# Kernel optimization log

Measured on AMD Instinct MI355X. Metric: run time of the kernel, lower is better.

## Reference

```python
import jax, jax.numpy as jnp
import numpy as np

B, TOK, NT = 64, 64, 456          # batch, token_encoder_dim, num gene tokens
T = NT * TOK                      # flat gene_exp dim = 29184
D, H, NL = 256, 8, 4              # d_model, nhead, num_layers
HD = D // H                       # head_dim = 32
FF = 4 * D                        # ffn hidden
PH = 32                           # attention-pooling hidden
L = NT + 1                        # seq len incl. CLS token
LN_EPS = 1e-5
BN_EPS = 1e-5


def build_alibi_slopes(n_heads):
    # faithful to FlashAttentionBlock.build_alibi_slopes (base=2.0)
    return jnp.array([1.0 / 2.0 ** (i // (n_heads / 2.0)) for i in range(n_heads)],
                     dtype=jnp.float32)


def _ln(x, g, b):
    m = jnp.mean(x, axis=-1, keepdims=True)
    v = jnp.mean(jnp.square(x - m), axis=-1, keepdims=True)
    return (x - m) * jax.lax.rsqrt(v + LN_EPS) * g + b


def setup_inputs() -> dict:
    key = jax.random.key(0)
    ks = jax.random.split(key, 24)
    s = 0.02
    return {
        "gene_exp": jax.random.normal(ks[0], (B, T), dtype=jnp.float32),
        "coords": jax.random.normal(ks[1], (B, 3), dtype=jnp.float32),
        "w_in": jax.random.normal(ks[2], (TOK, D)) * s,
        "b_in": jnp.zeros((D,), jnp.float32),
        "w_cls": jax.random.normal(ks[3], (3, D)) * s,
        "b_cls": jnp.zeros((D,), jnp.float32),
        "qkv_w": jax.random.normal(ks[4], (NL, D, 3 * D)) * s,
        "qkv_b": jnp.zeros((NL, 3 * D), jnp.float32),
        "ln1_g": jnp.ones((NL, D), jnp.float32),
        "ln1_b": jnp.zeros((NL, D), jnp.float32),
        "ffn_w1": jax.random.normal(ks[5], (NL, D, FF)) * s,
        "ffn_b1": jnp.zeros((NL, FF), jnp.float32),
        "ffn_w2": jax.random.normal(ks[6], (NL, FF, D)) * s,
        "ffn_b2": jnp.zeros((NL, D), jnp.float32),
        "ln2_g": jnp.ones((NL, D), jnp.float32),
        "ln2_b": jnp.zeros((NL, D), jnp.float32),
        "th1_w": jax.random.normal(ks[7], (D, PH)) * s,
        "th1_b": jnp.zeros((PH,), jnp.float32),
        "bn_g": jnp.ones((PH,), jnp.float32),
        "bn_b": jnp.zeros((PH,), jnp.float32),
        "th2_w": jax.random.normal(ks[8], (PH, 1)) * s,
        "th2_b": jnp.zeros((1,), jnp.float32),
    }


def reference(gene_exp, coords, w_in, b_in, w_cls, b_cls, qkv_w, qkv_b,
              ln1_g, ln1_b, ffn_w1, ffn_b1, ffn_w2, ffn_b2, ln2_g, ln2_b,
              th1_w, th1_b, bn_g, bn_b, th2_w, th2_b):
    # tokenize gene expression + project
    x = gene_exp.reshape(B, NT, TOK) @ w_in + b_in            # [B, NT, D]
    cls = (coords @ w_cls + b_cls)[:, None, :]                # [B, 1, D]
    x = jnp.concatenate([cls, x], axis=1)                     # [B, L, D]

    # ALiBi bias: -slope_h * |i - j| (non-causal flash-attn convention)
    slopes = build_alibi_slopes(H)                            # [H]
    pos = jnp.arange(L, dtype=jnp.float32)
    bias = -slopes[:, None, None] * jnp.abs(pos[:, None] - pos[None, :])  # [H,L,L]

    scale = 1.0 / np.sqrt(HD)
    for l in range(NL):
        residual = x
        qkv = (x @ qkv_w[l] + qkv_b[l]).reshape(B, L, 3, H, HD)
        q, k, v = qkv[:, :, 0], qkv[:, :, 1], qkv[:, :, 2]    # [B, L, H, HD]
        scores = jnp.einsum('bihd,bjhd->bhij', q, k) * scale + bias
        attn = jax.nn.softmax(scores, axis=-1)                # [B, H, L, L]
        out = jnp.einsum('bhij,bjhd->bihd', attn, v).reshape(B, L, D)
        x = _ln(residual + out, ln1_g[l], ln1_b[l])
        residual = x
        h = jax.nn.relu(x @ ffn_w1[l] + ffn_b1[l]) @ ffn_w2[l] + ffn_b2[l]
        x = _ln(residual + h, ln2_g[l], ln2_b[l])

    # AttentionPooling (BatchNorm1d in eval mode: running mean 0, var 1)
    h = x @ th1_w + th1_b                                     # [B, L, PH]
    h = h * (bn_g / np.sqrt(1.0 + BN_EPS)) + bn_b
    scores = jax.nn.gelu(h) @ th2_w + th2_b                   # [B, L, 1]
    attn_w = jax.nn.softmax(scores, axis=1)[..., 0]           # [B, L]
    pooled = jnp.einsum('bl,bld->bd', attn_w, x)              # [B, D]
    return pooled
```

## Files before the change

kernel.cpp:

```cpp
#include <hip/hip_runtime.h>
#include <math.h>

#define B_   64
#define TOK_ 64
#define NT_  456
#define L_   457
#define D_   256
#define H_   8
#define HD_  32
#define FF_  1024
#define NL_  4
#define PH_  32
#define MPAD 29440

typedef unsigned int uint;
typedef unsigned short ushort;
typedef __bf16 v8bf __attribute__((ext_vector_type(8)));
typedef __bf16 v4bf __attribute__((ext_vector_type(4)));
typedef short v4s __attribute__((ext_vector_type(4)));
typedef float v4f __attribute__((ext_vector_type(4)));

__device__ __forceinline__ float bu2f(ushort x) {
    return __uint_as_float(((uint)x) << 16);
}
__device__ __forceinline__ ushort f2bu(float f) {
    union { float f; uint u; } x; x.f = f;
    uint r = (x.u + 0x7fffu + ((x.u >> 16) & 1u)) >> 16;
    return (ushort)r;
}
__device__ __forceinline__ uint pack_bf2(float a, float b) {
#if defined(__HIP_DEVICE_COMPILE__) && __has_builtin(__builtin_amdgcn_cvt_pk_bf16_f32)
    typedef __bf16 bf2v __attribute__((ext_vector_type(2)));
    bf2v v = __builtin_amdgcn_cvt_pk_bf16_f32(a, b);
    return *(uint*)&v;
#else
    return (uint)f2bu(a) | ((uint)f2bu(b) << 16);
#endif
}

__device__ __forceinline__ v4f mfma16(uint2 a, uint2 b, v4f c) {
#if defined(__HIP_DEVICE_COMPILE__)
#if __has_builtin(__builtin_amdgcn_mfma_f32_16x16x16_bf16)
    return __builtin_amdgcn_mfma_f32_16x16x16_bf16(*(v4bf*)&a, *(v4bf*)&b, c, 0, 0, 0);
#else
    return __builtin_amdgcn_mfma_f32_16x16x16bf16_1k(*(v4s*)&a, *(v4s*)&b, c, 0, 0, 0);
#endif
#else
    (void)a; (void)b;
    return c;
#endif
}

__device__ __forceinline__ void gload16(const void* g, void* l) {
    __builtin_amdgcn_global_load_lds(
        (const __attribute__((address_space(1))) void*)(unsigned long long)(uintptr_t)g,
        (__attribute__((address_space(3))) void*)(uint)(uintptr_t)l,
        16, 0, 0);
}

__global__ __launch_bounds__(512, 2) void mfma_gemm8(
    const ushort* __restrict__ A, const ushort* __restrict__ WT,
    const float* __restrict__ bias, ushort* __restrict__ Cout,
    int N, int K, int relu)
{
    __shared__ ushort lds[36864];

    const int NK = K >> 5;

    int nwg = gridDim.x, orig = blockIdx.x;
    int qd = nwg >> 3, rd = nwg & 7;
    int xcd = orig & 7, wi = orig >> 3;
    int wgid = (xcd < rd ? xcd * (qd + 1) : rd * (qd + 1) + (xcd - rd) * qd) + wi;
    int nCB = N >> 7;
    int colblk = (wgid % nCB) << 7;
    int rowblk = (wgid / nCB) << 8;

    int tid = threadIdx.x;
    int wave = tid >> 6, lane = tid & 63;
    int wm = wave >> 1, wn = wave & 1;
    int fr = lane & 15, fq = lane >> 4;

    const ushort* srcA0; const ushort* srcA1; const ushort* srcB0;
    {
        int idx = tid;
        int c = idx >> 3, G = (idx & 7) ^ (c & 7);
        srcA0 = A + (size_t)(rowblk + c * 2 + (G >> 2)) * K + (G & 3) * 8;
        idx = 512 + tid;
        c = idx >> 3; G = (idx & 7) ^ (c & 7);
        srcA1 = A + (size_t)(rowblk + c * 2 + (G >> 2)) * K + (G & 3) * 8;
        idx = tid;
        c = idx >> 3; G = (idx & 7) ^ (c & 7);
        srcB0 = WT + (size_t)(colblk + c * 2 + (G >> 2)) * K + (G & 3) * 8;
    }
    int duA0 = (wave * 64) * 8;
    int duA1 = (512 + wave * 64) * 8;
    int duB  = (wave * 64) * 8;

    int aoff[4], boff[4];
#pragma unroll
    for (int i = 0; i < 4; ++i) {
        int rl = wm * 64 + i * 16 + fr;
        int c = rl >> 1;
        aoff[i] = c * 64 + ((((rl & 1) * 4 + fq) ^ (c & 7)) * 8);
        rl = wn * 64 + i * 16 + fr;
        c = rl >> 1;
        boff[i] = c * 64 + ((((rl & 1) * 4 + fq) ^ (c & 7)) * 8);
    }

    v4f acc[4][4];
#pragma unroll
    for (int i = 0; i < 4; ++i)
#pragma unroll
        for (int j = 0; j < 4; ++j) acc[i][j] = (v4f)0.0f;

#pragma unroll
    for (int t = 0; t < 2; ++t) {
        ushort* pa = lds + t * 8192;
        ushort* pb = lds + 24576 + t * 4096;
        gload16(srcA0 + t * 32, pa + duA0);
        gload16(srcA1 + t * 32, pa + duA1);
        gload16(srcB0 + t * 32, pb + duB);
    }

    for (int t = 0; t < NK; ++t) {
        int slot = t % 3, pslot = (t + 2) % 3;
        const ushort* As = lds + slot * 8192;
        const ushort* Bs = lds + 24576 + slot * 4096;

        if (t < NK - 1) asm volatile("s_waitcnt vmcnt(3)" ::: "memory");
        else            asm volatile("s_waitcnt vmcnt(0)" ::: "memory");
        __builtin_amdgcn_s_barrier();
        asm volatile("" ::: "memory");

        if (t + 2 < NK) {
            ushort* pa = lds + pslot * 8192;
            ushort* pb = lds + 24576 + pslot * 4096;
            gload16(srcA0 + (t + 2) * 32, pa + duA0);
            gload16(srcA1 + (t + 2) * 32, pa + duA1);
            gload16(srcB0 + (t + 2) * 32, pb + duB);
        }

        v8bf av[4], bw[4];
#pragma unroll
        for (int i = 0; i < 4; ++i) av[i] = *(const v8bf*)(As + aoff[i]);
#pragma unroll
        for (int i = 0; i < 4; ++i) bw[i] = *(const v8bf*)(Bs + boff[i]);

        __builtin_amdgcn_s_setprio(1);
#pragma unroll
        for (int mi = 0; mi < 4; ++mi)
#pragma unroll
            for (int ni = 0; ni < 4; ++ni)
                acc[mi][ni] = __builtin_amdgcn_mfma_f32_16x16x32_bf16(
                    av[mi], bw[ni], acc[mi][ni], 0, 0, 0);
        __builtin_amdgcn_s_setprio(0);
    }

    __syncthreads();
    {
        const int PIT = 136;
#pragma unroll
        for (int ni = 0; ni < 4; ++ni) {
            int col = wn * 64 + ni * 16 + fr;
            float bv = bias[colblk + col];
#pragma unroll
            for (int mi = 0; mi < 4; ++mi) {
                int row0 = wm * 64 + mi * 16 + fq * 4;
#pragma unroll
                for (int r2 = 0; r2 < 4; ++r2) {
                    float v = acc[mi][ni][r2] + bv;
                    if (relu) v = fmaxf(v, 0.f);
                    lds[(row0 + r2) * PIT + col] = f2bu(v);
                }
            }
        }
        __syncthreads();
#pragma unroll
        for (int i = 0; i < 8; ++i) {
            int u = tid + 512 * i;
            int row = u >> 4, c8 = (u & 15) * 8;
            uint4 val = *(const uint4*)&lds[row * PIT + c8];
            *(uint4*)(Cout + (size_t)(rowblk + row) * N + colblk + c8) = val;
        }
    }
}

__global__ __launch_bounds__(512, 4) void ffn_kernel(
    const ushort* __restrict__ Xres, const ushort* __restrict__ AO,
    const float* __restrict__ l1g, const float* __restrict__ l1b,
    const ushort* __restrict__ W1P, const ushort* __restrict__ W2P,
    const float* __restrict__ b1, const float* __restrict__ b2,
    const float* __restrict__ l2g, const float* __restrict__ l2b,
    ushort* __restrict__ Xout)
{
    __shared__ ushort Xs[16384];
    __shared__ ushort Hs[64 * 264];

    int r0 = blockIdx.x * 64;
    int tid = threadIdx.x;
    int wave = tid >> 6, lane = tid & 63;
    int fr = lane & 15, fq = lane >> 4;

    {
        float4 g1 = *(const float4*)(l1g + lane * 4);
        float4 be1 = *(const float4*)(l1b + lane * 4);
        ushort4 xr[8], ar[8];
#pragma unroll
        for (int rr = 0; rr < 8; ++rr) {
            size_t off = (size_t)(r0 + wave * 8 + rr) * 256 + lane * 4;
            xr[rr] = *(const ushort4*)(Xres + off);
            ar[rr] = *(const ushort4*)(AO + off);
        }
#pragma unroll
        for (int rr = 0; rr < 8; ++rr) {
            int row = wave * 8 + rr;
            float4 v;
            v.x = bu2f(xr[rr].x) + bu2f(ar[rr].x);
            v.y = bu2f(xr[rr].y) + bu2f(ar[rr].y);
            v.z = bu2f(xr[rr].z) + bu2f(ar[rr].z);
            v.w = bu2f(xr[rr].w) + bu2f(ar[rr].w);
            float s = v.x + v.y + v.z + v.w;
#pragma unroll
            for (int o = 1; o < 64; o <<= 1) s += __shfl_xor(s, o);
            float mean = s * (1.0f / 256.0f);
            float4 d;
            d.x = v.x - mean; d.y = v.y - mean; d.z = v.z - mean; d.w = v.w - mean;
            float sq = d.x * d.x + d.y * d.y + d.z * d.z + d.w * d.w;
#pragma unroll
            for (int o = 1; o < 64; o <<= 1) sq += __shfl_xor(sq, o);
            float rstd = rsqrtf(sq * (1.0f / 256.0f) + 1e-5f);
            ushort4 hb;
            hb.x = f2bu(d.x * rstd * g1.x + be1.x);
            hb.y = f2bu(d.y * rstd * g1.y + be1.y);
            hb.z = f2bu(d.z * rstd * g1.z + be1.z);
            hb.w = f2bu(d.w * rstd * g1.w + be1.w);
            int kt = lane >> 3, g = (lane >> 1) & 3, c = row >> 1;
            int Gp = ((row & 1) * 4 + g) ^ (c & 7);
            int addr = kt * 2048 + (c * 8 + Gp) * 8 + (lane & 1) * 4;
            *(uint2*)&Xs[addr] = *(uint2*)&hb;
        }
    }

    int aoffs[4];
#pragma unroll
    for (int mi = 0; mi < 4; ++mi) {
        int ar2 = mi * 16 + fr, c = ar2 >> 1;
        aoffs[mi] = c * 64 + ((((ar2 & 1) * 4 + fq) ^ (c & 7)) * 8);
    }
    int wm2 = wave >> 2, wn2 = wave & 3;

    v4f acc2[2][4];
#pragma unroll
    for (int i = 0; i < 2; ++i)
#pragma unroll
        for (int j = 0; j < 4; ++j) acc2[i][j] = (v4f)0.0f;

    __syncthreads();

#pragma unroll
    for (int q = 0; q < 4; ++q) {
        v4f acc1[4][2];
#pragma unroll
        for (int i = 0; i < 4; ++i)
#pragma unroll
            for (int j = 0; j < 2; ++j) acc1[i][j] = (v4f)0.0f;

        const ushort* w1p = W1P + (size_t)((q * 16 + wave * 2) * 8) * 64 * 8;
#pragma unroll
        for (int kc = 0; kc < 8; ++kc) {
            v8bf bf0 = *(const v8bf*)(w1p + ((size_t)kc * 64 + lane) * 8);
            v8bf bf1 = *(const v8bf*)(w1p + ((size_t)(8 + kc) * 64 + lane) * 8);
            v8bf a[4];
#pragma unroll
            for (int mi = 0; mi < 4; ++mi)
                a[mi] = *(const v8bf*)(Xs + kc * 2048 + aoffs[mi]);
#pragma unroll
            for (int mi = 0; mi < 4; ++mi) {
                acc1[mi][0] = __builtin_amdgcn_mfma_f32_16x16x32_bf16(
                    a[mi], bf0, acc1[mi][0], 0, 0, 0);
                acc1[mi][1] = __builtin_amdgcn_mfma_f32_16x16x32_bf16(
                    a[mi], bf1, acc1[mi][1], 0, 0, 0);
            }
        }
        float b1v[2];
#pragma unroll
        for (int ni = 0; ni < 2; ++ni)
            b1v[ni] = b1[q * 256 + wave * 32 + ni * 16 + fr];

        if (q) __syncthreads();
#pragma unroll
        for (int ni = 0; ni < 2; ++ni) {
            int col = wave * 32 + ni * 16 + fr;
#pragma unroll
            for (int mi = 0; mi < 4; ++mi) {
                int row0 = mi * 16 + fq * 4;
#pragma unroll
                for (int r2 = 0; r2 < 4; ++r2)
                    Hs[(row0 + r2) * 264 + col] =
                        f2bu(fmaxf(acc1[mi][ni][r2] + b1v[ni], 0.f));
            }
        }
        __syncthreads();

#pragma unroll
        for (int kk = 0; kk < 8; ++kk) {
            v8bf bw2[4];
#pragma unroll
            for (int ni = 0; ni < 4; ++ni)
                bw2[ni] = *(const v8bf*)(W2P +
                    (size_t)((((wn2 * 4 + ni) * 32 + q * 8 + kk) * 64 + lane)) * 8);
            v8bf a2[2];
#pragma unroll
            for (int mi = 0; mi < 2; ++mi)
                a2[mi] = *(const v8bf*)(Hs +
                    (wm2 * 32 + mi * 16 + fr) * 264 + kk * 32 + fq * 8);
#pragma unroll
            for (int mi = 0; mi < 2; ++mi)
#pragma unroll
                for (int ni = 0; ni < 4; ++ni)
                    acc2[mi][ni] = __builtin_amdgcn_mfma_f32_16x16x32_bf16(
                        a2[mi], bw2[ni], acc2[mi][ni], 0, 0, 0);
        }
    }

    __syncthreads();
    {
        float b2v[4];
#pragma unroll
        for (int ni = 0; ni < 4; ++ni) b2v[ni] = b2[wn2 * 64 + ni * 16 + fr];
#pragma unroll
        for (int ni = 0; ni < 4; ++ni) {
            int col = wn2 * 64 + ni * 16 + fr;
#pragma unroll
            for (int mi = 0; mi < 2; ++mi) {
                int row0 = wm2 * 32 + mi * 16 + fq * 4;
#pragma unroll
                for (int r2 = 0; r2 < 4; ++r2)
                    Hs[(row0 + r2) * 264 + col] = f2bu(acc2[mi][ni][r2] + b2v[ni]);
            }
        }
        __syncthreads();

        float4 g2 = *(const float4*)(l2g + lane * 4);
        float4 be2 = *(const float4*)(l2b + lane * 4);
#pragma unroll
        for (int rr = 0; rr < 8; ++rr) {
            int row = wave * 8 + rr;
            ushort4 cv = *(const ushort4*)&Hs[row * 264 + lane * 4];
            int kt = lane >> 3, g = (lane >> 1) & 3, c = row >> 1;
            int Gp = ((row & 1) * 4 + g) ^ (c & 7);
            int addr = kt * 2048 + (c * 8 + Gp) * 8 + (lane & 1) * 4;
            uint2 uu = *(const uint2*)&Xs[addr];
            ushort4 uv = *(ushort4*)&uu;
            float4 v;
            v.x = bu2f(cv.x) + bu2f(uv.x);
            v.y = bu2f(cv.y) + bu2f(uv.y);
            v.z = bu2f(cv.z) + bu2f(uv.z);
            v.w = bu2f(cv.w) + bu2f(uv.w);
            float s = v.x + v.y + v.z + v.w;
#pragma unroll
            for (int o = 1; o < 64; o <<= 1) s += __shfl_xor(s, o);
            float mean = s * (1.0f / 256.0f);
            float4 d;
            d.x = v.x - mean; d.y = v.y - mean; d.z = v.z - mean; d.w = v.w - mean;
            float sq = d.x * d.x + d.y * d.y + d.z * d.z + d.w * d.w;
#pragma unroll
            for (int o = 1; o < 64; o <<= 1) sq += __shfl_xor(sq, o);
            float rstd = rsqrtf(sq * (1.0f / 256.0f) + 1e-5f);
            ushort4 hb;
            hb.x = f2bu(d.x * rstd * g2.x + be2.x);
            hb.y = f2bu(d.y * rstd * g2.y + be2.y);
            hb.z = f2bu(d.z * rstd * g2.z + be2.z);
            hb.w = f2bu(d.w * rstd * g2.w + be2.w);
            *(ushort4*)(Xout + (size_t)(r0 + row) * 256 + lane * 4) = hb;
        }
    }
}

__global__ __launch_bounds__(256) void wpack_kernel(
    const float* __restrict__ W, ushort* __restrict__ P, int K, int N)
{
    int KC = K >> 5;
    int total = (N >> 4) * KC * 64;
    const float* Wl = W + (size_t)blockIdx.z * K * N;
    ushort* Pl = P + (size_t)blockIdx.z * K * N;
    int gid = blockIdx.x * 256 + threadIdx.x;
    if (gid >= total) return;
    int lane = gid & 63;
    int t = gid >> 6;
    int kc = t % KC, grp = t / KC;
    int n = grp * 16 + (lane & 15);
    int k0 = kc * 32 + (lane >> 4) * 8;
    float v[8];
#pragma unroll
    for (int e = 0; e < 8; ++e) v[e] = Wl[(size_t)(k0 + e) * N + n];
    uint4 o;
    o.x = pack_bf2(v[0], v[1]);
    o.y = pack_bf2(v[2], v[3]);
    o.z = pack_bf2(v[4], v[5]);
    o.w = pack_bf2(v[6], v[7]);
    *(uint4*)&Pl[(size_t)gid * 8] = o;
}

__global__ __launch_bounds__(256) void wcast_kernel(
    const float* __restrict__ W, ushort* __restrict__ WT, int K, int N)
{
    __shared__ float t[32][33];
    const float* Wl = W + (size_t)blockIdx.z * K * N;
    ushort* WTl = WT + (size_t)blockIdx.z * K * N;
    int n0 = blockIdx.x * 32, k0 = blockIdx.y * 32;
    int tx = threadIdx.x, ty = threadIdx.y;
#pragma unroll
    for (int r = 0; r < 32; r += 8)
        t[ty + r][tx] = Wl[(size_t)(k0 + ty + r) * N + n0 + tx];
    __syncthreads();
#pragma unroll
    for (int r = 0; r < 32; r += 8)
        WTl[(size_t)(n0 + ty + r) * K + k0 + tx] = f2bu(t[tx][ty + r]);
}

__global__ __launch_bounds__(256) void sgemm_kernel(
    const float* __restrict__ A, const float* __restrict__ W,
    const float* __restrict__ bias, ushort* __restrict__ Cb,
    int M, int N, int K)
{
    __shared__ float As_[16][64];
    __shared__ float Bs_[16][64];
    int tid = threadIdx.x;
    int rowblk = blockIdx.y * 64;
    int colblk = blockIdx.x * 64;
    int a_row = tid & 63, a_q = tid >> 6;
    int b_kr = tid >> 4, b_cg = tid & 15;
    int rm = tid >> 4, cn = tid & 15;
    float acc[4][4] = {};
    const float* Aptr = A + (size_t)(rowblk + a_row) * K;
    for (int kt = 0; kt < K; kt += 16) {
        float4 av = *(const float4*)(Aptr + kt + a_q * 4);
        float4 bv = *(const float4*)(W + (size_t)(kt + b_kr) * N + colblk + b_cg * 4);
        As_[a_q * 4 + 0][a_row] = av.x;
        As_[a_q * 4 + 1][a_row] = av.y;
        As_[a_q * 4 + 2][a_row] = av.z;
        As_[a_q * 4 + 3][a_row] = av.w;
        *(float4*)&Bs_[b_kr][b_cg * 4] = bv;
        __syncthreads();
#pragma unroll
        for (int kk = 0; kk < 16; ++kk) {
            float4 a4 = *(const float4*)&As_[kk][rm * 4];
            float4 b4 = *(const float4*)&Bs_[kk][cn * 4];
            float ar[4] = {a4.x, a4.y, a4.z, a4.w};
            float br[4] = {b4.x, b4.y, b4.z, b4.w};
#pragma unroll
            for (int i = 0; i < 4; ++i)
#pragma unroll
                for (int j = 0; j < 4; ++j) acc[i][j] += ar[i] * br[j];
        }
        __syncthreads();
    }
    float4 bv = *(const float4*)(bias + colblk + cn * 4);
    float bb[4] = {bv.x, bv.y, bv.z, bv.w};
#pragma unroll
    for (int i = 0; i < 4; ++i) {
        int grow = rowblk + rm * 4 + i;
        size_t orow = (size_t)(grow + grow / NT_ + 1);
        ushort4 h;
        h.x = f2bu(acc[i][0] + bb[0]);
        h.y = f2bu(acc[i][1] + bb[1]);
        h.z = f2bu(acc[i][2] + bb[2]);
        h.w = f2bu(acc[i][3] + bb[3]);
        *(ushort4*)(Cb + orow * N + colblk + cn * 4) = h;
    }
}

__global__ __launch_bounds__(256) void cls_kernel(
    const float* __restrict__ coords, const float* __restrict__ w_cls,
    const float* __restrict__ b_cls, ushort* __restrict__ Xb)
{
    int b = blockIdx.x;
    int t = threadIdx.x;
    float c0 = coords[b * 3 + 0], c1 = coords[b * 3 + 1], c2 = coords[b * 3 + 2];
    float v = c0 * w_cls[t] + c1 * w_cls[D_ + t] + c2 * w_cls[2 * D_ + t] + b_cls[t];
    Xb[(size_t)b * L_ * D_ + t] = f2bu(v);
}

__global__ __launch_bounds__(512) void attn_kernel(
    const ushort* __restrict__ qkv, ushort* __restrict__ out)
{
    __shared__ __align__(16) ushort Ks[464][40];
    __shared__ __align__(16) ushort Vt[32][488];

    int h = blockIdx.x, b = blockIdx.y;
    int tid = threadIdx.x;
    int wave = tid >> 6, lane = tid & 63;
    int fr = lane & 15, fq = lane >> 4;
    const float scale2 = 0.17677669529663687f * 1.4426950408889634f;
    float slope2 = ((h < 4) ? 1.0f : 0.5f) * 1.4426950408889634f;
    int W = (h < 4) ? 32 : 64;
    const ushort* base = qkv + (size_t)b * L_ * 768;

    for (int j = tid >> 2; j < 464; j += 128) {
        int c8 = (tid & 3) * 8;
        uint4 u = make_uint4(0u, 0u, 0u, 0u);
        if (j < L_) u = *(const uint4*)(base + (size_t)j * 768 + 256 + h * 32 + c8);
        *(uint4*)&Ks[j][c8] = u;
    }
    for (int m = wave; m < 32; m += 8) {
        int dg = (m >> 3) * 8, jb = m & 7;
        int j = jb * 64 + lane;
        uint4 u = make_uint4(0u, 0u, 0u, 0u);
        if (j < L_) u = *(const uint4*)(base + (size_t)j * 768 + 512 + h * 32 + dg);
        if (j < 488) {
            const ushort* pu = (const ushort*)&u;
#pragma unroll
            for (int e = 0; e < 8; ++e) Vt[dg + e][j] = pu[e];
        }
    }
    __syncthreads();

    for (int pr = wave; pr < 15; pr += 8) {
        int q0 = pr * 32;
        int twoB = (pr < 14);
        int kclo = max(0, (q0 - W) >> 5);
        int kchi = min(13, (q0 + 31 + W) >> 5);
        int doTail = (q0 + 31 + W >= 448);
        uint4 quA = *(const uint4*)(base + (size_t)(q0 + fr) * 768 + h * 32 + fq * 8);
        v8bf qfA = *(v8bf*)&quA;
        uint4 quB = *(const uint4*)(base + (size_t)(q0 + 16 + fr) * 768 + h * 32 + fq * 8);
        v8bf qfB = *(v8bf*)&quB;
        float fqAq = (float)(q0 + fr);
        float fqBq = fqAq + 16.0f;
        float psA = 0.f, psB = 0.f;
        v4f oA0 = (v4f)0.0f, oA1 = (v4f)0.0f, oB0 = (v4f)0.0f, oB1 = (v4f)0.0f;

        for (int kc = kclo; kc <= kchi; ++kc) {
            int kb = kc * 32;
            v8bf kf0 = *(const v8bf*)&Ks[kb + fr][fq * 8];
            v8bf kf1 = *(const v8bf*)&Ks[kb + 16 + fr][fq * 8];
            uint2 va0 = *(const uint2*)&Vt[fr][kb + fq * 4];
            uint2 va1 = *(const uint2*)&Vt[16 + fr][kb + fq * 4];
            uint2 vb0 = *(const uint2*)&Vt[fr][kb + 16 + fq * 4];
            uint2 vb1 = *(const uint2*)&Vt[16 + fr][kb + 16 + fq * 4];
            float ke = (float)(kb + 4 * fq);

            v4f dA0 = (v4f)0.0f, dA1 = (v4f)0.0f;
            dA0 = __builtin_amdgcn_mfma_f32_16x16x32_bf16(kf0, qfA, dA0, 0, 0, 0);
            dA1 = __builtin_amdgcn_mfma_f32_16x16x32_bf16(kf1, qfA, dA1, 0, 0, 0);
            {
                float dl0 = fqAq - ke, dl1 = dl0 - 16.0f;
                float pe[4], po[4];
#pragma unroll
                for (int r = 0; r < 4; ++r) {
                    pe[r] = exp2f(fmaf(dA0[r], scale2, -slope2 * fabsf(dl0 - (float)r)));
                    po[r] = exp2f(fmaf(dA1[r], scale2, -slope2 * fabsf(dl1 - (float)r)));
                    psA += pe[r] + po[r];
                }
                uint2 ue, uo;
                ue.x = pack_bf2(pe[0], pe[1]); ue.y = pack_bf2(pe[2], pe[3]);
                uo.x = pack_bf2(po[0], po[1]); uo.y = pack_bf2(po[2], po[3]);
                oA0 = mfma16(va0, ue, oA0);
                oA1 = mfma16(va1, ue, oA1);
                oA0 = mfma16(vb0, uo, oA0);
                oA1 = mfma16(vb1, uo, oA1);
            }
            if (twoB) {
                v4f dB0 = (v4f)0.0f, dB1 = (v4f)0.0f;
                dB0 = __builtin_amdgcn_mfma_f32_16x16x32_bf16(kf0, qfB, dB0, 0, 0, 0);
                dB1 = __builtin_amdgcn_mfma_f32_16x16x32_bf16(kf1, qfB, dB1, 0, 0, 0);
                float dl0 = fqBq - ke, dl1 = dl0 - 16.0f;
                float pe[4], po[4];
#pragma unroll
                for (int r = 0; r < 4; ++r) {
                    pe[r] = exp2f(fmaf(dB0[r], scale2, -slope2 * fabsf(dl0 - (float)r)));
                    po[r] = exp2f(fmaf(dB1[r], scale2, -slope2 * fabsf(dl1 - (float)r)));
                    psB += pe[r] + po[r];
                }
                uint2 ue, uo;
                ue.x = pack_bf2(pe[0], pe[1]); ue.y = pack_bf2(pe[2], pe[3]);
                uo.x = pack_bf2(po[0], po[1]); uo.y = pack_bf2(po[2], po[3]);
                oB0 = mfma16(va0, ue, oB0);
                oB1 = mfma16(va1, ue, oB1);
                oB0 = mfma16(vb0, uo, oB0);
                oB1 = mfma16(vb1, uo, oB1);
            }
        }
        if (doTail) {
            v8bf kf0 = *(const v8bf*)&Ks[448 + fr][fq * 8];
            uint2 va0 = *(const uint2*)&Vt[fr][448 + fq * 4];
            uint2 va1 = *(const uint2*)&Vt[16 + fr][448 + fq * 4];
            v4f dA0 = (v4f)0.0f;
            dA0 = __builtin_amdgcn_mfma_f32_16x16x32_bf16(kf0, qfA, dA0, 0, 0, 0);
            float pe[4];
#pragma unroll
            for (int r = 0; r < 4; ++r) {
                int k = 448 + 4 * fq + r;
                pe[r] = (k < L_)
                    ? exp2f(fmaf(dA0[r], scale2, -slope2 * fabsf(fqAq - (float)k))) : 0.f;
                psA += pe[r];
            }
            uint2 ue;
            ue.x = pack_bf2(pe[0], pe[1]); ue.y = pack_bf2(pe[2], pe[3]);
            oA0 = mfma16(va0, ue, oA0);
            oA1 = mfma16(va1, ue, oA1);
            if (twoB) {
                v4f dB0 = (v4f)0.0f;
                dB0 = __builtin_amdgcn_mfma_f32_16x16x32_bf16(kf0, qfB, dB0, 0, 0, 0);
                float pf[4];
#pragma unroll
                for (int r = 0; r < 4; ++r) {
                    int k = 448 + 4 * fq + r;
                    pf[r] = (k < L_)
                        ? exp2f(fmaf(dB0[r], scale2, -slope2 * fabsf(fqBq - (float)k))) : 0.f;
                    psB += pf[r];
                }
                uint2 ub;
                ub.x = pack_bf2(pf[0], pf[1]); ub.y = pack_bf2(pf[2], pf[3]);
                oB0 = mfma16(va0, ub, oB0);
                oB1 = mfma16(va1, ub, oB1);
            }
        }

        psA += __shfl_xor(psA, 16);
        psA += __shfl_xor(psA, 32);
        psB += __shfl_xor(psB, 16);
        psB += __shfl_xor(psB, 32);
        {
            int q = q0 + fr;
            if (q < L_) {
                float inv = 1.0f / psA;
                uint2 w0, w1;
                w0.x = pack_bf2(oA0[0] * inv, oA0[1] * inv);
                w0.y = pack_bf2(oA0[2] * inv, oA0[3] * inv);
                w1.x = pack_bf2(oA1[0] * inv, oA1[1] * inv);
                w1.y = pack_bf2(oA1[2] * inv, oA1[3] * inv);
                ushort* op = out + (size_t)(b * L_ + q) * D_ + h * 32;
                *(uint2*)(op + fq * 4) = w0;
                *(uint2*)(op + 16 + fq * 4) = w1;
            }
        }
        if (twoB) {
            int q = q0 + 16 + fr;
            if (q < L_) {
                float inv = 1.0f / psB;
                uint2 w0, w1;
                w0.x = pack_bf2(oB0[0] * inv, oB0[1] * inv);
                w0.y = pack_bf2(oB0[2] * inv, oB0[3] * inv);
                w1.x = pack_bf2(oB1[0] * inv, oB1[1] * inv);
                w1.y = pack_bf2(oB1[2] * inv, oB1[3] * inv);
                ushort* op = out + (size_t)(b * L_ + q) * D_ + h * 32;
                *(uint2*)(op + fq * 4) = w0;
                *(uint2*)(op + 16 + fq * 4) = w1;
            }
        }
    }
}

__global__ __launch_bounds__(256) void head1_kernel(
    const ushort* __restrict__ Xb, const ushort* __restrict__ th1T,
    const float* __restrict__ b1, const float* __restrict__ bng,
    const float* __restrict__ bnb, const float* __restrict__ w2,
    const float* __restrict__ b2, float* __restrict__ SCp)
{
    __shared__ ushort As[128 * 32];
    __shared__ ushort Bs[32 * 264];
    int tid = threadIdx.x;
    int wave = tid >> 6, lane = tid & 63;
    int fr = lane & 15, fq = lane >> 4;
    int rowblk = blockIdx.x * 128;
    int scol = fq ^ (lane & 3) ^ ((lane >> 2) & 1);

    for (int i = tid; i < 1024; i += 256) {
        int r = i >> 5, c8 = (i & 31) * 8;
        *(uint4*)&Bs[r * 264 + c8] = *(const uint4*)(th1T + r * 256 + c8);
    }

    int c0 = wave * 64 + lane;
    int r0 = c0 >> 2, k0g = (c0 & 3) ^ (r0 & 3) ^ ((r0 >> 2) & 1);
    int c1 = 256 + c0;
    int r1 = c1 >> 2, k1g = (c1 & 3) ^ (r1 & 3) ^ ((r1 >> 2) & 1);
    const ushort* Ag0 = Xb + (size_t)(rowblk + r0) * 256 + k0g * 8;
    const ushort* Ag1 = Xb + (size_t)(rowblk + r1) * 256 + k1g * 8;
    ushort* lA0 = As + (size_t)(wave * 64) * 8;
    ushort* lA1 = As + (size_t)(256 + wave * 64) * 8;

    v4f acc[2][2];
#pragma unroll
    for (int i = 0; i < 2; ++i)
#pragma unroll
        for (int j = 0; j < 2; ++j) acc[i][j] = (v4f)0.0f;

    for (int kt = 0; kt < 256; kt += 32) {
        gload16(Ag0 + kt, lA0);
        gload16(Ag1 + kt, lA1);
        __syncthreads();
        v8bf a[2], bfr[2];
#pragma unroll
        for (int mi = 0; mi < 2; ++mi)
            a[mi] = *(const v8bf*)(As + (size_t)((wave * 2 + mi) * 16 + fr) * 32 + scol * 8);
#pragma unroll
        for (int ni = 0; ni < 2; ++ni)
            bfr[ni] = *(const v8bf*)(Bs + (size_t)(ni * 16 + fr) * 264 + kt + fq * 8);
#pragma unroll
        for (int mi = 0; mi < 2; ++mi)
#pragma unroll
            for (int ni = 0; ni < 2; ++ni)
                acc[mi][ni] = __builtin_amdgcn_mfma_f32_16x16x32_bf16(
                    a[mi], bfr[ni], acc[mi][ni], 0, 0, 0);
        __syncthreads();
    }

    const float bnr = 0.9999950000374997f;
    float b1v[2], bsv[2], bbv[2], w2v[2];
#pragma unroll
    for (int ni = 0; ni < 2; ++ni) {
        int j = ni * 16 + fr;
        b1v[ni] = b1[j];
        bsv[ni] = bng[j] * bnr;
        bbv[ni] = bnb[j];
        w2v[ni] = w2[j];
    }
    const float gc = 0.7978845608028654f;
    float b2v = b2[0];
#pragma unroll
    for (int mi = 0; mi < 2; ++mi) {
#pragma unroll
        for (int r = 0; r < 4; ++r) {
            float s = 0.f;
#pragma unroll
            for (int ni = 0; ni < 2; ++ni) {
                float hb = (acc[mi][ni][r] + b1v[ni]) * bsv[ni] + bbv[ni];
                float t = tanhf(gc * (hb + 0.044715f * hb * hb * hb));
                s += 0.5f * hb * (1.0f + t) * w2v[ni];
            }
#pragma unroll
            for (int o = 1; o < 16; o <<= 1) s += __shfl_xor(s, o);
            int row = rowblk + (wave * 2 + mi) * 16 + fq * 4 + r;
            if (fr == 0 && row < B_ * L_) SCp[row] = s + b2v;
        }
    }
}

__global__ __launch_bounds__(256) void head2_kernel(
    const float* __restrict__ SCp, const ushort* __restrict__ Xb,
    float* __restrict__ outp)
{
    int cg = blockIdx.x, b = blockIdx.y;
    int tid = threadIdx.x;
    __shared__ float wbuf[L_];
    __shared__ float r1[4], r2[4];
    __shared__ float part[4][64];
    const float* s = SCp + (size_t)b * L_;

    float m = -1e30f;
    for (int j = tid; j < L_; j += 256) m = fmaxf(m, s[j]);
#pragma unroll
    for (int o = 1; o < 64; o <<= 1) m = fmaxf(m, __shfl_xor(m, o));
    if ((tid & 63) == 0) r1[tid >> 6] = m;
    __syncthreads();
    m = fmaxf(fmaxf(r1[0], r1[1]), fmaxf(r1[2], r1[3]));

    float sum = 0.f;
    for (int j = tid; j < L_; j += 256) {
        float e = __expf(s[j] - m);
        wbuf[j] = e;
        sum += e;
    }
#pragma unroll
    for (int o = 1; o < 64; o <<= 1) sum += __shfl_xor(sum, o);
    if ((tid & 63) == 0) r2[tid >> 6] = sum;
    __syncthreads();
    float inv = 1.0f / (r2[0] + r2[1] + r2[2] + r2[3]);

    int c = tid & 63, pt = tid >> 6;
    int col = cg * 64 + c;
    float acc = 0.f;
    const ushort* xb = Xb + (size_t)b * L_ * D_ + col;
    for (int l = pt; l < L_; l += 4) acc += wbuf[l] * bu2f(xb[(size_t)l * D_]);
    part[pt][c] = acc;
    __syncthreads();
    if (pt == 0)
        outp[b * D_ + col] = (part[0][c] + part[1][c] + part[2][c] + part[3][c]) * inv;
}

extern "C" void kernel_launch(void* const* d_in, const int* in_sizes, int n_in,
                              void* d_out, int out_size, void* d_ws, size_t ws_size,
                              hipStream_t stream)
{
    const float* gene   = (const float*)d_in[0];
    const float* coords = (const float*)d_in[1];
    const float* w_in   = (const float*)d_in[2];
    const float* b_in   = (const float*)d_in[3];
    const float* w_cls  = (const float*)d_in[4];
    const float* b_cls  = (const float*)d_in[5];
    const float* qkv_w  = (const float*)d_in[6];
    const float* qkv_b  = (const float*)d_in[7];
    const float* ln1_g  = (const float*)d_in[8];
    const float* ln1_b  = (const float*)d_in[9];
    const float* ffn_w1 = (const float*)d_in[10];
    const float* ffn_b1 = (const float*)d_in[11];
    const float* ffn_w2 = (const float*)d_in[12];
    const float* ffn_b2 = (const float*)d_in[13];
    const float* ln2_g  = (const float*)d_in[14];
    const float* ln2_b  = (const float*)d_in[15];
    const float* th1_w  = (const float*)d_in[16];
    const float* th1_b  = (const float*)d_in[17];
    const float* bn_g   = (const float*)d_in[18];
    const float* bn_b   = (const float*)d_in[19];
    const float* th2_w  = (const float*)d_in[20];
    const float* th2_b  = (const float*)d_in[21];
    float* out = (float*)d_out;

    const int ROWS = B_ * L_;
    char* p = (char*)d_ws;
    ushort* AOb  = (ushort*)p; p += (size_t)MPAD * 256 * 2;
    ushort* Xb   = (ushort*)p; p += (size_t)MPAD * 256 * 2;
    ushort* SH   = (ushort*)p; p += (size_t)MPAD * 1024 * 2;
    ushort* qkvT = (ushort*)p; p += (size_t)NL_ * 768 * 256 * 2;
    ushort* W1P  = (ushort*)p; p += (size_t)NL_ * 1024 * 256 * 2;
    ushort* W2P  = (ushort*)p; p += (size_t)NL_ * 256 * 1024 * 2;
    ushort* th1T = (ushort*)p; p += (size_t)32 * 256 * 2;
    float*  SCp  = (float*)p;  p += (size_t)ROWS * 4;

    const int RB2 = MPAD / 256;

    wcast_kernel<<<dim3(768 / 32, 256 / 32, NL_), dim3(32, 8), 0, stream>>>(qkv_w, qkvT, 256, 768);
    wpack_kernel<<<dim3(128, 1, NL_), 256, 0, stream>>>(ffn_w1, W1P, 256, 1024);
    wpack_kernel<<<dim3(128, 1, NL_), 256, 0, stream>>>(ffn_w2, W2P, 1024, 256);
    wcast_kernel<<<dim3(1, 8, 1), dim3(32, 8), 0, stream>>>(th1_w, th1T, 256, 32);

    sgemm_kernel<<<dim3(D_ / 64, (B_ * NT_) / 64), 256, 0, stream>>>(
        gene, w_in, b_in, Xb, B_ * NT_, D_, TOK_);
    cls_kernel<<<B_, 256, 0, stream>>>(coords, w_cls, b_cls, Xb);

    for (int l = 0; l < NL_; ++l) {
        mfma_gemm8<<<RB2 * (768 / 128), 512, 0, stream>>>(
            Xb, qkvT + (size_t)l * 768 * 256, qkv_b + l * 768, SH, 768, 256, 0);
        attn_kernel<<<dim3(H_, B_), 512, 0, stream>>>(SH, AOb);
        ffn_kernel<<<MPAD / 64, 512, 0, stream>>>(
            Xb, AOb, ln1_g + l * D_, ln1_b + l * D_,
            W1P + (size_t)l * 1024 * 256, W2P + (size_t)l * 256 * 1024,
            ffn_b1 + l * 1024, ffn_b2 + l * D_,
            ln2_g + l * D_, ln2_b + l * D_, Xb);
    }

    head1_kernel<<<MPAD / 128, 256, 0, stream>>>(
        Xb, th1T, th1_b, bn_g, bn_b, th2_w, th2_b, SCp);
    head2_kernel<<<dim3(4, B_), 256, 0, stream>>>(SCp, Xb, out);
}
```

Before: 627.2 us.

## Halve FFN hidden chunk and LDS footprint to raise occupancy

```diff
diff --git a/kernel.cpp b/kernel.cpp
--- a/kernel.cpp
+++ b/kernel.cpp
@@ -185,7 +185,7 @@
     }
 }
 
-__global__ __launch_bounds__(512, 4) void ffn_kernel(
+__global__ __launch_bounds__(512, 6) void ffn_kernel(
     const ushort* __restrict__ Xres, const ushort* __restrict__ AO,
     const float* __restrict__ l1g, const float* __restrict__ l1b,
     const ushort* __restrict__ W1P, const ushort* __restrict__ W2P,
@@ -194,13 +194,14 @@
     ushort* __restrict__ Xout)
 {
     __shared__ ushort Xs[16384];
-    __shared__ ushort Hs[64 * 264];
+    __shared__ ushort Hs[64 * 132];
 
     int r0 = blockIdx.x * 64;
     int tid = threadIdx.x;
     int wave = tid >> 6, lane = tid & 63;
     int fr = lane & 15, fq = lane >> 4;
 
+    uint2 ur[8];
     {
         float4 g1 = *(const float4*)(l1g + lane * 4);
         float4 be1 = *(const float4*)(l1b + lane * 4);
@@ -234,10 +235,11 @@
             hb.y = f2bu(d.y * rstd * g1.y + be1.y);
             hb.z = f2bu(d.z * rstd * g1.z + be1.z);
             hb.w = f2bu(d.w * rstd * g1.w + be1.w);
+            ur[rr] = *(uint2*)&hb;
             int kt = lane >> 3, g = (lane >> 1) & 3, c = row >> 1;
             int Gp = ((row & 1) * 4 + g) ^ (c & 7);
             int addr = kt * 2048 + (c * 8 + Gp) * 8 + (lane & 1) * 4;
-            *(uint2*)&Xs[addr] = *(uint2*)&hb;
+            *(uint2*)&Xs[addr] = ur[rr];
         }
     }
 
@@ -258,62 +260,47 @@
     __syncthreads();
 
 #pragma unroll
-    for (int q = 0; q < 4; ++q) {
-        v4f acc1[4][2];
-#pragma unroll
-        for (int i = 0; i < 4; ++i)
-#pragma unroll
-            for (int j = 0; j < 2; ++j) acc1[i][j] = (v4f)0.0f;
-
-        const ushort* w1p = W1P + (size_t)((q * 16 + wave * 2) * 8) * 64 * 8;
+    for (int e = 0; e < 8; ++e) {
+        v4f acc1[4];
+#pragma unroll
+        for (int i = 0; i < 4; ++i) acc1[i] = (v4f)0.0f;
+
+        const ushort* w1p = W1P + ((size_t)(e * 8 + wave) * 8) * 512;
 #pragma unroll
         for (int kc = 0; kc < 8; ++kc) {
-            v8bf bf0 = *(const v8bf*)(w1p + ((size_t)kc * 64 + lane) * 8);
-            v8bf bf1 = *(const v8bf*)(w1p + ((size_t)(8 + kc) * 64 + lane) * 8);
-            v8bf a[4];
-#pragma unroll
-            for (int mi = 0; mi < 4; ++mi)
-                a[mi] = *(const v8bf*)(Xs + kc * 2048 + aoffs[mi]);
+            v8bf bf0 = *(const v8bf*)(w1p + (size_t)kc * 512 + lane * 8);
 #pragma unroll
             for (int mi = 0; mi < 4; ++mi) {
-                acc1[mi][0] = __builtin_amdgcn_mfma_f32_16x16x32_bf16(
-                    a[mi], bf0, acc1[mi][0], 0, 0, 0);
-                acc1[mi][1] = __builtin_amdgcn_mfma_f32_16x16x32_bf16(
-                    a[mi], bf1, acc1[mi][1], 0, 0, 0);
-            }
-        }
-        float b1v[2];
-#pragma unroll
-        for (int ni = 0; ni < 2; ++ni)
-            b1v[ni] = b1[q * 256 + wave * 32 + ni * 16 + fr];
-
-        if (q) __syncthreads();
-#pragma unroll
-        for (int ni = 0; ni < 2; ++ni) {
-            int col = wave * 32 + ni * 16 + fr;
-#pragma unroll
-            for (int mi = 0; mi < 4; ++mi) {
-                int row0 = mi * 16 + fq * 4;
-#pragma unroll
-                for (int r2 = 0; r2 < 4; ++r2)
-                    Hs[(row0 + r2) * 264 + col] =
-                        f2bu(fmaxf(acc1[mi][ni][r2] + b1v[ni], 0.f));
-            }
+                v8bf a = *(const v8bf*)(Xs + kc * 2048 + aoffs[mi]);
+                acc1[mi] = __builtin_amdgcn_mfma_f32_16x16x32_bf16(
+                    a, bf0, acc1[mi], 0, 0, 0);
+            }
+        }
+        float b1v = b1[e * 128 + wave * 16 + fr];
+
+        if (e) __syncthreads();
+#pragma unroll
+        for (int mi = 0; mi < 4; ++mi) {
+            int row0 = mi * 16 + fq * 4;
+#pragma unroll
+            for (int r2 = 0; r2 < 4; ++r2)
+                Hs[(row0 + r2) * 132 + wave * 16 + fr] =
+                    f2bu(fmaxf(acc1[mi][r2] + b1v, 0.f));
         }
         __syncthreads();
 
 #pragma unroll
-        for (int kk = 0; kk < 8; ++kk) {
+        for (int kk = 0; kk < 4; ++kk) {
             v8bf bw2[4];
 #pragma unroll
             for (int ni = 0; ni < 4; ++ni)
                 bw2[ni] = *(const v8bf*)(W2P +
-                    (size_t)((((wn2 * 4 + ni) * 32 + q * 8 + kk) * 64 + lane)) * 8);
+                    ((size_t)(((wn2 * 4 + ni) * 32 + e * 4 + kk)) * 512) + lane * 8);
             v8bf a2[2];
 #pragma unroll
             for (int mi = 0; mi < 2; ++mi)
                 a2[mi] = *(const v8bf*)(Hs +
-                    (wm2 * 32 + mi * 16 + fr) * 264 + kk * 32 + fq * 8);
+                    (wm2 * 32 + mi * 16 + fr) * 132 + kk * 32 + fq * 8);
 #pragma unroll
             for (int mi = 0; mi < 2; ++mi)
 #pragma unroll
@@ -335,8 +322,11 @@
             for (int mi = 0; mi < 2; ++mi) {
                 int row0 = wm2 * 32 + mi * 16 + fq * 4;
 #pragma unroll
-                for (int r2 = 0; r2 < 4; ++r2)
-                    Hs[(row0 + r2) * 264 + col] = f2bu(acc2[mi][ni][r2] + b2v[ni]);
+                for (int r2 = 0; r2 < 4; ++r2) {
+                    ushort cvb = f2bu(acc2[mi][ni][r2] + b2v[ni]);
+                    if (wn2 < 2) Hs[(row0 + r2) * 132 + col] = cvb;
+                    else         Xs[(row0 + r2) * 136 + col - 128] = cvb;
+                }
             }
         }
         __syncthreads();
@@ -346,12 +336,10 @@
 #pragma unroll
         for (int rr = 0; rr < 8; ++rr) {
             int row = wave * 8 + rr;
-            ushort4 cv = *(const ushort4*)&Hs[row * 264 + lane * 4];
-            int kt = lane >> 3, g = (lane >> 1) & 3, c = row >> 1;
-            int Gp = ((row & 1) * 4 + g) ^ (c & 7);
-            int addr = kt * 2048 + (c * 8 + Gp) * 8 + (lane & 1) * 4;
-            uint2 uu = *(const uint2*)&Xs[addr];
-            ushort4 uv = *(ushort4*)&uu;
+            ushort4 cv;
+            if (lane < 32) cv = *(const ushort4*)&Hs[row * 132 + lane * 4];
+            else           cv = *(const ushort4*)&Xs[row * 136 + lane * 4 - 128];
+            ushort4 uv = *(ushort4*)&ur[rr];
             float4 v;
             v.x = bu2f(cv.x) + bu2f(uv.x);
             v.y = bu2f(cv.y) + bu2f(uv.y);
```

After: 738.9 us. 17.8% more time.
